# Performance work log

Hardware: AMD Instinct MI355X
Metric: run time of the kernel (lower is better)

The kernel has to match this reference:

```python
import jax, jax.numpy as jnp
import numpy as np

TOP_K = 8
N_HEADS = 16


def setup_inputs() -> dict:
    key = jax.random.key(0)
    ks = jax.random.split(key, 8)
    B, L, S, D = 8, 1024, 1024, 1024
    w_scale = 1.0 / np.sqrt(D)
    return {
        "queries": jax.random.normal(ks[0], (B, L, D), jnp.float32),
        "keys": jax.random.normal(ks[1], (B, S, D), jnp.float32),
        "values": jax.random.normal(ks[2], (B, S, D), jnp.float32),
        "Wq": jax.random.normal(ks[3], (D, D), jnp.float32) * w_scale,
        "bq": jnp.zeros((D,), jnp.float32),
        "Wk": jax.random.normal(ks[4], (D, D), jnp.float32) * w_scale,
        "bk": jnp.zeros((D,), jnp.float32),
        "Wv": jax.random.normal(ks[5], (D, D), jnp.float32) * w_scale,
        "bv": jnp.zeros((D,), jnp.float32),
        "Wo": jax.random.normal(ks[6], (D, D), jnp.float32) * w_scale,
        "bo": jnp.zeros((D,), jnp.float32),
    }


def reference(queries, keys, values, Wq, bq, Wk, bk, Wv, bv, Wo, bo):
    B, L, D = queries.shape
    S = keys.shape[1]
    H = N_HEADS
    E = D // H
    # projections (torch Linear: x @ W.T + b); relu on Q and V per source
    q = jax.nn.relu(queries @ Wq.T + bq).reshape(B, L, H, E)
    k = (keys @ Wk.T + bk).reshape(B, S, H, E)
    v = jax.nn.relu(values @ Wv.T + bv).reshape(B, S, H, E)
    scores = jnp.einsum('blhe,bshe->bhls', q, k)  # [B,H,L,S]
    # per-row top-k threshold; entries strictly below kth-largest masked to -inf
    thresh = jax.lax.top_k(scores, TOP_K)[0][..., -1:]
    masked = jnp.where(scores < thresh, -jnp.inf, scores)
    scale = 1.0 / np.sqrt(E)
    A = jax.nn.softmax(scale * masked, axis=-1)  # dropout p=0.0 -> identity
    V = jnp.einsum('bhls,bshd->blhd', A, v).reshape(B, L, D)
    out = V @ Wo.T + bo
    return out, A
```

## Files before the change

kernel.cpp:

```cpp
#include <hip/hip_runtime.h>
#include <hip/hip_bf16.h>


#define B_ 8
#define L_ 1024
#define S_ 1024
#define D_ 1024
#define H_ 16
#define E_ 64
#define TOPK_ 8

typedef __attribute__((ext_vector_type(8))) short bfrag8;
typedef __attribute__((ext_vector_type(4))) float f4acc;

__device__ __forceinline__ void gload_lds16(const float* g, float* l) {
  __builtin_amdgcn_global_load_lds(
      (const __attribute__((address_space(1))) unsigned int*)g,
      (__attribute__((address_space(3))) unsigned int*)l, 16, 0, 0);
}

__device__ __forceinline__ unsigned short f2bf(float f) {
  unsigned u = __float_as_uint(f);
  u += 0x7FFF + ((u >> 16) & 1);
  return (unsigned short)(u >> 16);
}

__device__ __forceinline__ unsigned enc_ord(float f) {
  int s = __float_as_int(f);
  return (unsigned)(s ^ ((s >> 31) | 0x80000000));
}
__device__ __forceinline__ float dec_ord(unsigned u) {
  int m = ((int)u >= 0) ? 0xFFFFFFFF : 0x80000000;
  return __int_as_float((int)(u ^ (unsigned)m));
}

__device__ __forceinline__ unsigned dpp_umax64(unsigned x) {
  unsigned t;
  t = (unsigned)__builtin_amdgcn_update_dpp((int)x, (int)x, 0x111, 0xf, 0xf, false);
  x = x > t ? x : t;
  t = (unsigned)__builtin_amdgcn_update_dpp((int)x, (int)x, 0x112, 0xf, 0xf, false);
  x = x > t ? x : t;
  t = (unsigned)__builtin_amdgcn_update_dpp((int)x, (int)x, 0x114, 0xf, 0xf, false);
  x = x > t ? x : t;
  t = (unsigned)__builtin_amdgcn_update_dpp((int)x, (int)x, 0x118, 0xf, 0xf, false);
  x = x > t ? x : t;
  t = (unsigned)__builtin_amdgcn_update_dpp((int)x, (int)x, 0x142, 0xa, 0xf, false);
  x = x > t ? x : t;
  t = (unsigned)__builtin_amdgcn_update_dpp((int)x, (int)x, 0x143, 0xc, 0xf, false);
  x = x > t ? x : t;
  return (unsigned)__builtin_amdgcn_readlane((int)x, 63);
}

__device__ __forceinline__ float dpp_fsum64(float x) {
  float t;
  t = __int_as_float(__builtin_amdgcn_update_dpp(0, __float_as_int(x), 0x111, 0xf, 0xf, true));
  x += t;
  t = __int_as_float(__builtin_amdgcn_update_dpp(0, __float_as_int(x), 0x112, 0xf, 0xf, true));
  x += t;
  t = __int_as_float(__builtin_amdgcn_update_dpp(0, __float_as_int(x), 0x114, 0xf, 0xf, true));
  x += t;
  t = __int_as_float(__builtin_amdgcn_update_dpp(0, __float_as_int(x), 0x118, 0xf, 0xf, true));
  x += t;
  t = __int_as_float(__builtin_amdgcn_update_dpp(0, __float_as_int(x), 0x142, 0xa, 0xf, true));
  x += t;
  t = __int_as_float(__builtin_amdgcn_update_dpp(0, __float_as_int(x), 0x143, 0xc, 0xf, true));
  x += t;
  return __int_as_float(__builtin_amdgcn_readlane(__float_as_int(x), 63));
}

template <int RELU>
__global__ __launch_bounds__(256) void gemm_abt(
    const float* __restrict__ A, const float* __restrict__ Bm,
    const float* __restrict__ bias, float* __restrict__ C,
    int M, int N, int K, int lda, int ldb, int ldc) {
  __shared__ float As[2][16][68];
  __shared__ float Bs[2][16][68];

  const int t = threadIdx.x;
  const int tx = t & 15, ty = t >> 4;
  const int m0 = blockIdx.y * 64, n0 = blockIdx.x * 64;
  const int sr = t >> 2, skq = (t & 3) * 4;

  float acc[4][4], tot[4][4];
#pragma unroll
  for (int r = 0; r < 4; ++r)
#pragma unroll
    for (int c = 0; c < 4; ++c) {
      acc[r][c] = 0.0f;
      tot[r][c] = 0.0f;
    }

  const float* Arow = A + (long long)(m0 + sr) * lda + skq;
  const float* Brow = Bm + (long long)(n0 + sr) * ldb + skq;

  float4 pa = *reinterpret_cast<const float4*>(Arow);
  float4 pb = *reinterpret_cast<const float4*>(Brow);
  {
    As[0][skq + 0][sr] = pa.x;
    As[0][skq + 1][sr] = pa.y;
    As[0][skq + 2][sr] = pa.z;
    As[0][skq + 3][sr] = pa.w;
    Bs[0][skq + 0][sr] = pb.x;
    Bs[0][skq + 1][sr] = pb.y;
    Bs[0][skq + 2][sr] = pb.z;
    Bs[0][skq + 3][sr] = pb.w;
  }
  __syncthreads();

  const int ntiles = K / 16;
  for (int ti = 0; ti < ntiles; ++ti) {
    const int cur = ti & 1, nxt = cur ^ 1;
    if (ti + 1 < ntiles) {
      pa = *reinterpret_cast<const float4*>(Arow + (ti + 1) * 16);
      pb = *reinterpret_cast<const float4*>(Brow + (ti + 1) * 16);
    }
#pragma unroll
    for (int kk = 0; kk < 16; ++kk) {
      const float4 a4 = *reinterpret_cast<const float4*>(&As[cur][kk][ty * 4]);
      const float4 b4 = *reinterpret_cast<const float4*>(&Bs[cur][kk][tx * 4]);
      const float av[4] = {a4.x, a4.y, a4.z, a4.w};
      const float bv[4] = {b4.x, b4.y, b4.z, b4.w};
#pragma unroll
      for (int r = 0; r < 4; ++r)
#pragma unroll
        for (int c = 0; c < 4; ++c) acc[r][c] = fmaf(av[r], bv[c], acc[r][c]);
    }
    if (ti + 1 < ntiles) {
      As[nxt][skq + 0][sr] = pa.x;
      As[nxt][skq + 1][sr] = pa.y;
      As[nxt][skq + 2][sr] = pa.z;
      As[nxt][skq + 3][sr] = pa.w;
      Bs[nxt][skq + 0][sr] = pb.x;
      Bs[nxt][skq + 1][sr] = pb.y;
      Bs[nxt][skq + 2][sr] = pb.z;
      Bs[nxt][skq + 3][sr] = pb.w;
    }
    const bool flush =
        (K == 1024) ? (ti == 31 || ti == 63) : (ti == ntiles - 1);
    if (flush) {
#pragma unroll
      for (int r = 0; r < 4; ++r)
#pragma unroll
        for (int c = 0; c < 4; ++c) {
          tot[r][c] = __fadd_rn(tot[r][c], acc[r][c]);
          acc[r][c] = 0.0f;
        }
    }
    __syncthreads();
  }

#pragma unroll
  for (int r = 0; r < 4; ++r) {
    const int m = m0 + ty * 4 + r;
#pragma unroll
    for (int c = 0; c < 4; ++c) {
      const int n = n0 + tx * 4 + c;
      float v = tot[r][c];
      if (bias) v = __fadd_rn(v, bias[n]);
      if (RELU) v = fmaxf(v, 0.0f);
      C[(long long)m * ldc + n] = v;
    }
  }
}

template <int RELU>
__global__ __launch_bounds__(256) void gemm_mfma(
    const float* __restrict__ A, const float* __restrict__ Bm,
    const float* __restrict__ bias, float* __restrict__ C,
    int M, int N, int K, int lda, int ldb, int ldc) {
  __shared__ unsigned short As[2][64][40];
  __shared__ unsigned short Bs[2][64][40];

  const int t = threadIdx.x;
  const int w = t >> 6, l = t & 63;
  const int lr = l & 15, lg = l >> 4;
  const int m0 = blockIdx.y * 64, n0 = blockIdx.x * 64;
  const int srow = t >> 2, scol = (t & 3) * 8;

  f4acc acc[4];
#pragma unroll
  for (int c = 0; c < 4; ++c) acc[c] = (f4acc){0.f, 0.f, 0.f, 0.f};

  const float* Arow = A + (long long)(m0 + srow) * lda + scol;
  const float* Brow = Bm + (long long)(n0 + srow) * ldb + scol;

  float4 pa0 = *reinterpret_cast<const float4*>(Arow);
  float4 pa1 = *reinterpret_cast<const float4*>(Arow + 4);
  float4 pb0 = *reinterpret_cast<const float4*>(Brow);
  float4 pb1 = *reinterpret_cast<const float4*>(Brow + 4);

  auto store_tile = [&](int buf, const float4& a0, const float4& a1,
                        const float4& b0, const float4& b1) {
    unsigned short* ap = &As[buf][srow][scol];
    ap[0] = f2bf(a0.x); ap[1] = f2bf(a0.y); ap[2] = f2bf(a0.z);
    ap[3] = f2bf(a0.w); ap[4] = f2bf(a1.x); ap[5] = f2bf(a1.y);
    ap[6] = f2bf(a1.z); ap[7] = f2bf(a1.w);
    unsigned short* bp = &Bs[buf][srow][scol];
    bp[0] = f2bf(b0.x); bp[1] = f2bf(b0.y); bp[2] = f2bf(b0.z);
    bp[3] = f2bf(b0.w); bp[4] = f2bf(b1.x); bp[5] = f2bf(b1.y);
    bp[6] = f2bf(b1.z); bp[7] = f2bf(b1.w);
  };

  store_tile(0, pa0, pa1, pb0, pb1);
  __syncthreads();

  const int nsteps = K / 32;
  for (int ks = 0; ks < nsteps; ++ks) {
    const int cur = ks & 1, nxt = cur ^ 1;
    if (ks + 1 < nsteps) {
      const int off = (ks + 1) * 32;
      pa0 = *reinterpret_cast<const float4*>(Arow + off);
      pa1 = *reinterpret_cast<const float4*>(Arow + off + 4);
      pb0 = *reinterpret_cast<const float4*>(Brow + off);
      pb1 = *reinterpret_cast<const float4*>(Brow + off + 4);
    }
    const bfrag8 av =
        *reinterpret_cast<const bfrag8*>(&As[cur][16 * w + lr][lg * 8]);
#pragma unroll
    for (int c = 0; c < 4; ++c) {
      const bfrag8 bv =
          *reinterpret_cast<const bfrag8*>(&Bs[cur][16 * c + lr][lg * 8]);
      acc[c] = __builtin_amdgcn_mfma_f32_16x16x32_bf16(av, bv, acc[c], 0, 0, 0);
    }
    if (ks + 1 < nsteps) store_tile(nxt, pa0, pa1, pb0, pb1);
    __syncthreads();
  }

#pragma unroll
  for (int c = 0; c < 4; ++c) {
    const int col = n0 + c * 16 + lr;
    const float bb = bias ? bias[col] : 0.0f;
#pragma unroll
    for (int j = 0; j < 4; ++j) {
      const int row = m0 + 16 * w + lg * 4 + j;
      float v = acc[c][j] + bb;
      if (RELU) v = fmaxf(v, 0.0f);
      C[(long long)row * ldc + col] = v;
    }
  }
}

__global__ __launch_bounds__(256) void transpose_k(const float* __restrict__ Kf,
                                                   float* __restrict__ Kt) {
  __shared__ float tl[64][65];
  const int bh = blockIdx.y;
  const int b = bh >> 4, h = bh & 15;
  const int s0 = blockIdx.x * 64;
  const int t = threadIdx.x;
#pragma unroll
  for (int i = 0; i < 16; ++i) {
    const int idx = i * 256 + t;
    const int sr = idx >> 6, e = idx & 63;
    tl[sr][e] = Kf[(((long long)(b << 10) + s0 + sr) << 10) + (h << 6) + e];
  }
  __syncthreads();
#pragma unroll
  for (int i = 0; i < 16; ++i) {
    const int idx = i * 256 + t;
    const int er = idx >> 6, s = idx & 63;
    Kt[(((long long)(bh << 6) + er) << 10) + s0 + s] = tl[s][er];
  }
}

__global__ __launch_bounds__(256, 4) void score_topk_fused(
    const float* __restrict__ Qf, const float* __restrict__ Kt,
    float* __restrict__ A, int* __restrict__ outIdx,
    float* __restrict__ outW, int* __restrict__ outCnt) {
#pragma clang fp contract(off)
  __shared__ float Ks[2][8][512];

  const int t = threadIdx.x;
  const int wv = t >> 6, u = t & 63;
  const int row0 = blockIdx.x * 16;
  const int b = row0 >> 14, h = (row0 >> 10) & 15;
  const int bh = (b << 4) + h;
  const int rbase = (row0 & 1023) + wv * 4;

  float qreg[4];
#pragma unroll
  for (int r = 0; r < 4; ++r)
    qreg[r] = Qf[(((long long)(b << 10) + rbase + r) << 10) + (h << 6) + u];

  const float* KtBase = Kt + ((long long)(bh << 6) << 10);

  float acc[4][16];
#pragma unroll
  for (int r = 0; r < 4; ++r)
#pragma unroll
    for (int j = 0; j < 16; ++j) acc[r][j] = 0.0f;

  auto stage = [&](int buf, int eo, int ch) {
    const int r0 = wv * 2;
#pragma unroll
    for (int i = 0; i < 2; ++i) {
      const float* src =
          KtBase + ((long long)(eo * 8 + r0 + i) << 10) + ch * 512;
      float* dst = &Ks[buf][r0 + i][0];
      gload_lds16(src + 4 * u, dst);
      gload_lds16(src + 256 + 4 * u, dst + 256);
    }
  };

  stage(0, 0, 0);
  __syncthreads();

  for (int eo = 0; eo < 8; ++eo) {
    float qv[8][4];
#pragma unroll
    for (int el = 0; el < 8; ++el)
#pragma unroll
      for (int r = 0; r < 4; ++r)
        qv[el][r] = __uint_as_float(__builtin_amdgcn_readlane(
            __float_as_uint(qreg[r]), eo * 8 + el));

    {
      stage(1, eo, 1);
#pragma unroll
      for (int el = 0; el < 8; ++el) {
        const float4 k0 = *reinterpret_cast<const float4*>(&Ks[0][el][4 * u]);
        const float4 k1 =
            *reinterpret_cast<const float4*>(&Ks[0][el][256 + 4 * u]);
#pragma unroll
        for (int r = 0; r < 4; ++r) {
          const float q = qv[el][r];
          acc[r][0] = fmaf(q, k0.x, acc[r][0]);
          acc[r][1] = fmaf(q, k0.y, acc[r][1]);
          acc[r][2] = fmaf(q, k0.z, acc[r][2]);
          acc[r][3] = fmaf(q, k0.w, acc[r][3]);
          acc[r][4] = fmaf(q, k1.x, acc[r][4]);
          acc[r][5] = fmaf(q, k1.y, acc[r][5]);
          acc[r][6] = fmaf(q, k1.z, acc[r][6]);
          acc[r][7] = fmaf(q, k1.w, acc[r][7]);
        }
      }
      __syncthreads();
    }
    {
      if (eo < 7) stage(0, eo + 1, 0);
#pragma unroll
      for (int el = 0; el < 8; ++el) {
        const float4 k0 = *reinterpret_cast<const float4*>(&Ks[1][el][4 * u]);
        const float4 k1 =
            *reinterpret_cast<const float4*>(&Ks[1][el][256 + 4 * u]);
#pragma unroll
        for (int r = 0; r < 4; ++r) {
          const float q = qv[el][r];
          acc[r][8] = fmaf(q, k0.x, acc[r][8]);
          acc[r][9] = fmaf(q, k0.y, acc[r][9]);
          acc[r][10] = fmaf(q, k0.z, acc[r][10]);
          acc[r][11] = fmaf(q, k0.w, acc[r][11]);
          acc[r][12] = fmaf(q, k1.x, acc[r][12]);
          acc[r][13] = fmaf(q, k1.y, acc[r][13]);
          acc[r][14] = fmaf(q, k1.z, acc[r][14]);
          acc[r][15] = fmaf(q, k1.w, acc[r][15]);
        }
      }
      __syncthreads();
    }
  }

  float T[4], cnt8[4], rowmax[4];
#pragma unroll
  for (int r = 0; r < 4; ++r) {
    T[r] = INFINITY;
    cnt8[r] = 0.0f;
    rowmax[r] = 0.0f;
  }

  for (int it = 0; it < TOPK_; ++it) {
    float m[4];
#pragma unroll
    for (int r = 0; r < 4; ++r) {
      float lm = -INFINITY;
#pragma unroll
      for (int j = 0; j < 16; ++j) {
        const float v = acc[r][j];
        lm = fmaxf(lm, v < T[r] ? v : -INFINITY);
      }
      m[r] = lm;
    }
    unsigned mu[4];
#pragma unroll
    for (int r = 0; r < 4; ++r) mu[r] = enc_ord(m[r]);
#pragma unroll
    for (int r = 0; r < 4; ++r) mu[r] = dpp_umax64(mu[r]);
#pragma unroll
    for (int r = 0; r < 4; ++r) m[r] = dec_ord(mu[r]);

    float nn[4];
#pragma unroll
    for (int r = 0; r < 4; ++r) {
      float cl = 0.0f;
#pragma unroll
      for (int j = 0; j < 16; ++j) cl += (acc[r][j] == m[r]) ? 1.0f : 0.0f;
      nn[r] = cl;
    }
#pragma unroll
    for (int r = 0; r < 4; ++r) nn[r] = dpp_fsum64(nn[r]);

#pragma unroll
    for (int r = 0; r < 4; ++r) {
      if (it == 0) rowmax[r] = m[r];
      const bool upd = (cnt8[r] < 8.0f);
      T[r] = upd ? m[r] : T[r];
      cnt8[r] = upd ? cnt8[r] + nn[r] : cnt8[r];
    }
  }

#pragma unroll
  for (int r = 0; r < 4; ++r) {
    const float thresh = T[r];
    float e16[16];
    float zl = 0.0f;
#pragma unroll
    for (int j = 0; j < 16; ++j) {
      const bool kept = (acc[r][j] >= thresh);
      const float e = kept ? __expf((acc[r][j] - rowmax[r]) * 0.125f) : 0.0f;
      e16[j] = e;
      zl += e;
    }
    const float zsum = dpp_fsum64(zl);
    const float inv = 1.0f / zsum;

    const long long row = row0 + wv * 4 + r;
    float* a = A + (row << 10);
    int cnt = 0;
#pragma unroll
    for (int j = 0; j < 16; ++j) {
      const bool kept = (acc[r][j] >= thresh);
      const float w = e16[j] * inv;
      e16[j] = kept ? w : 0.0f;
      const unsigned long long mk = __ballot(kept);
      if (kept) {
        const int pos = cnt + __popcll(mk & ((1ull << u) - 1ull));
        if (pos < 16) {
          const int col = (j >> 2) * 256 + 4 * u + (j & 3);
          outIdx[row * 16 + pos] = col;
          outW[row * 16 + pos] = w;
        }
      }
      cnt += __popcll(mk);
    }
    if (u == 0) outCnt[row] = cnt < 16 ? cnt : 16;

#pragma unroll
    for (int blkc = 0; blkc < 4; ++blkc) {
      float4 o;
      o.x = e16[blkc * 4 + 0];
      o.y = e16[blkc * 4 + 1];
      o.z = e16[blkc * 4 + 2];
      o.w = e16[blkc * 4 + 3];
      *reinterpret_cast<float4*>(&a[blkc * 256 + 4 * u]) = o;
    }
  }
}

__global__ __launch_bounds__(256) void vagg_kernel(
    const int* __restrict__ idx, const float* __restrict__ w,
    const int* __restrict__ cnt, const float* __restrict__ Vp,
    float* __restrict__ Vagg) {
  const int wave = threadIdx.x >> 6;
  const int lane = threadIdx.x & 63;
  const long long row = (long long)blockIdx.x * 4 + wave;
  const int b = (int)(row >> 14);
  const int h = (int)((row >> 10) & 15);
  const int l = (int)(row & 1023);
  const int n = cnt[row];
  float acc = 0.0f;
  for (int i = 0; i < n; ++i) {
    const int sI = idx[row * 16 + i];
    const float ww = w[row * 16 + i];
    acc += ww * Vp[((long long)((b << 10) + sI) << 10) + (h << 6) + lane];
  }
  Vagg[((long long)((b << 10) + l) << 10) + (h << 6) + lane] = acc;
}

extern "C" void kernel_launch(void* const* d_in, const int* in_sizes, int n_in,
                              void* d_out, int out_size, void* d_ws,
                              size_t ws_size, hipStream_t stream) {
  const float* queries = (const float*)d_in[0];
  const float* keys = (const float*)d_in[1];
  const float* values = (const float*)d_in[2];
  const float* Wq = (const float*)d_in[3];
  const float* bq = (const float*)d_in[4];
  const float* Wk = (const float*)d_in[5];
  const float* bk = (const float*)d_in[6];
  const float* Wv = (const float*)d_in[7];
  const float* bv = (const float*)d_in[8];
  const float* Wo = (const float*)d_in[9];
  const float* bo = (const float*)d_in[10];

  float* out = (float*)d_out;
  float* Aout = out + (long long)B_ * L_ * D_;

  char* ws = (char*)d_ws;
  const size_t MD = (size_t)B_ * L_ * D_ * sizeof(float);
  const size_t NL = (size_t)B_ * H_ * L_;
  float* Qf = (float*)ws;
  float* Kf = (float*)(ws + MD);
  float* Kt = (float*)(ws + 2 * MD);
  int* tIdx = (int*)(ws + 3 * MD);
  float* tW = (float*)(ws + 3 * MD + NL * 16 * 4);
  int* tCnt = (int*)(ws + 3 * MD + NL * 16 * 8);
  float* Vb = (float*)(ws + 3 * MD + NL * 16 * 8 + NL * 4);
  float* Vagg = Kt;

  const dim3 blk(256);
  const int M = B_ * L_;

  gemm_abt<1><<<dim3(16, M / 64), blk, 0, stream>>>(queries, Wq, bq, Qf, M, D_,
                                                    D_, D_, D_, D_);
  gemm_abt<0><<<dim3(16, M / 64), blk, 0, stream>>>(keys, Wk, bk, Kf, M, D_,
                                                    D_, D_, D_, D_);
  transpose_k<<<dim3(16, B_ * H_), blk, 0, stream>>>(Kf, Kt);

  score_topk_fused<<<(int)(NL / 16), blk, 0, stream>>>(Qf, Kt, Aout, tIdx, tW,
                                                       tCnt);

  gemm_mfma<1><<<dim3(16, M / 64), blk, 0, stream>>>(values, Wv, bv, Vb, M, D_,
                                                     D_, D_, D_, D_);

  vagg_kernel<<<(int)(NL / 4), blk, 0, stream>>>(tIdx, tW, tCnt, Vb, Vagg);

  gemm_mfma<0><<<dim3(16, M / 64), blk, 0, stream>>>(Vagg, Wo, bo, out, M, D_,
                                                     D_, D_, D_, D_);
}
```

Measured before the change: 1.213 ms.

## Fuse K transpose into projection GEMM epilogue and shrink score staging tiles

The key-projection GEMM now writes its output directly in the per-head transposed [B,H,E,S] layout through a templated epilogue using float4 stores. This removes the separate transpose kernel and one full-size intermediate buffer round trip. The score kernel's LDS staging is halved to 256-wide chunks in a four-step double-buffered loop with a fully unrolled outer loop, which lowers LDS use per block but adds more barriers. Vagg gets its own workspace region because Kt is no longer free to alias.

```diff
diff --git a/kernel.cpp b/kernel.cpp
--- a/kernel.cpp
+++ b/kernel.cpp
@@ -68,7 +68,7 @@
   return __int_as_float(__builtin_amdgcn_readlane(__float_as_int(x), 63));
 }
 
-template <int RELU>
+template <int RELU, int KT = 0>
 __global__ __launch_bounds__(256) void gemm_abt(
     const float* __restrict__ A, const float* __restrict__ Bm,
     const float* __restrict__ bias, float* __restrict__ C,
@@ -149,16 +149,33 @@
     __syncthreads();
   }
 
-#pragma unroll
-  for (int r = 0; r < 4; ++r) {
-    const int m = m0 + ty * 4 + r;
+  if (KT) {
+    const int bb = m0 >> 10;
+    const int sb = (m0 & 1023) + ty * 4;
 #pragma unroll
     for (int c = 0; c < 4; ++c) {
       const int n = n0 + tx * 4 + c;
-      float v = tot[r][c];
-      if (bias) v = __fadd_rn(v, bias[n]);
-      if (RELU) v = fmaxf(v, 0.0f);
-      C[(long long)m * ldc + n] = v;
+      const int hh = n >> 6, ee = n & 63;
+      float4 v;
+      v.x = __fadd_rn(tot[0][c], bias[n]);
+      v.y = __fadd_rn(tot[1][c], bias[n]);
+      v.z = __fadd_rn(tot[2][c], bias[n]);
+      v.w = __fadd_rn(tot[3][c], bias[n]);
+      *reinterpret_cast<float4*>(
+          &C[((((long long)(bb << 4) + hh) << 6) + ee) * 1024 + sb]) = v;
+    }
+  } else {
+#pragma unroll
+    for (int r = 0; r < 4; ++r) {
+      const int m = m0 + ty * 4 + r;
+#pragma unroll
+      for (int c = 0; c < 4; ++c) {
+        const int n = n0 + tx * 4 + c;
+        float v = tot[r][c];
+        if (bias) v = __fadd_rn(v, bias[n]);
+        if (RELU) v = fmaxf(v, 0.0f);
+        C[(long long)m * ldc + n] = v;
+      }
     }
   }
 }
@@ -240,34 +257,12 @@
   }
 }
 
-__global__ __launch_bounds__(256) void transpose_k(const float* __restrict__ Kf,
-                                                   float* __restrict__ Kt) {
-  __shared__ float tl[64][65];
-  const int bh = blockIdx.y;
-  const int b = bh >> 4, h = bh & 15;
-  const int s0 = blockIdx.x * 64;
-  const int t = threadIdx.x;
-#pragma unroll
-  for (int i = 0; i < 16; ++i) {
-    const int idx = i * 256 + t;
-    const int sr = idx >> 6, e = idx & 63;
-    tl[sr][e] = Kf[(((long long)(b << 10) + s0 + sr) << 10) + (h << 6) + e];
-  }
-  __syncthreads();
-#pragma unroll
-  for (int i = 0; i < 16; ++i) {
-    const int idx = i * 256 + t;
-    const int er = idx >> 6, s = idx & 63;
-    Kt[(((long long)(bh << 6) + er) << 10) + s0 + s] = tl[s][er];
-  }
-}
-
 __global__ __launch_bounds__(256, 4) void score_topk_fused(
     const float* __restrict__ Qf, const float* __restrict__ Kt,
     float* __restrict__ A, int* __restrict__ outIdx,
     float* __restrict__ outW, int* __restrict__ outCnt) {
 #pragma clang fp contract(off)
-  __shared__ float Ks[2][8][512];
+  __shared__ float Ks[2][8][256];
 
   const int t = threadIdx.x;
   const int wv = t >> 6, u = t & 63;
@@ -294,16 +289,15 @@
 #pragma unroll
     for (int i = 0; i < 2; ++i) {
       const float* src =
-          KtBase + ((long long)(eo * 8 + r0 + i) << 10) + ch * 512;
-      float* dst = &Ks[buf][r0 + i][0];
-      gload_lds16(src + 4 * u, dst);
-      gload_lds16(src + 256 + 4 * u, dst + 256);
+          KtBase + ((long long)(eo * 8 + r0 + i) << 10) + ch * 256 + 4 * u;
+      gload_lds16(src, &Ks[buf][r0 + i][0]);
     }
   };
 
   stage(0, 0, 0);
   __syncthreads();
 
+#pragma unroll
   for (int eo = 0; eo < 8; ++eo) {
     float qv[8][4];
 #pragma unroll
@@ -313,46 +307,24 @@
         qv[el][r] = __uint_as_float(__builtin_amdgcn_readlane(
             __float_as_uint(qreg[r]), eo * 8 + el));
 
-    {
-      stage(1, eo, 1);
+#pragma unroll
+    for (int ch = 0; ch < 4; ++ch) {
+      const int cur = ch & 1;
+      if (!(eo == 7 && ch == 3)) {
+        const int nch = (ch + 1) & 3;
+        const int neo = eo + (ch == 3 ? 1 : 0);
+        stage(cur ^ 1, neo, nch);
+      }
 #pragma unroll
       for (int el = 0; el < 8; ++el) {
-        const float4 k0 = *reinterpret_cast<const float4*>(&Ks[0][el][4 * u]);
-        const float4 k1 =
-            *reinterpret_cast<const float4*>(&Ks[0][el][256 + 4 * u]);
+        const float4 k4 = *reinterpret_cast<const float4*>(&Ks[cur][el][4 * u]);
 #pragma unroll
         for (int r = 0; r < 4; ++r) {
           const float q = qv[el][r];
-          acc[r][0] = fmaf(q, k0.x, acc[r][0]);
-          acc[r][1] = fmaf(q, k0.y, acc[r][1]);
-          acc[r][2] = fmaf(q, k0.z, acc[r][2]);
-          acc[r][3] = fmaf(q, k0.w, acc[r][3]);
-          acc[r][4] = fmaf(q, k1.x, acc[r][4]);
-          acc[r][5] = fmaf(q, k1.y, acc[r][5]);
-          acc[r][6] = fmaf(q, k1.z, acc[r][6]);
-          acc[r][7] = fmaf(q, k1.w, acc[r][7]);
-        }
-      }
-      __syncthreads();
-    }
-    {
-      if (eo < 7) stage(0, eo + 1, 0);
-#pragma unroll
-      for (int el = 0; el < 8; ++el) {
-        const float4 k0 = *reinterpret_cast<const float4*>(&Ks[1][el][4 * u]);
-        const float4 k1 =
-            *reinterpret_cast<const float4*>(&Ks[1][el][256 + 4 * u]);
-#pragma unroll
-        for (int r = 0; r < 4; ++r) {
-          const float q = qv[el][r];
-          acc[r][8] = fmaf(q, k0.x, acc[r][8]);
-          acc[r][9] = fmaf(q, k0.y, acc[r][9]);
-          acc[r][10] = fmaf(q, k0.z, acc[r][10]);
-          acc[r][11] = fmaf(q, k0.w, acc[r][11]);
-          acc[r][12] = fmaf(q, k1.x, acc[r][12]);
-          acc[r][13] = fmaf(q, k1.y, acc[r][13]);
-          acc[r][14] = fmaf(q, k1.z, acc[r][14]);
-          acc[r][15] = fmaf(q, k1.w, acc[r][15]);
+          acc[r][ch * 4 + 0] = fmaf(q, k4.x, acc[r][ch * 4 + 0]);
+          acc[r][ch * 4 + 1] = fmaf(q, k4.y, acc[r][ch * 4 + 1]);
+          acc[r][ch * 4 + 2] = fmaf(q, k4.z, acc[r][ch * 4 + 2]);
+          acc[r][ch * 4 + 3] = fmaf(q, k4.w, acc[r][ch * 4 + 3]);
         }
       }
       __syncthreads();
@@ -497,22 +469,20 @@
   const size_t MD = (size_t)B_ * L_ * D_ * sizeof(float);
   const size_t NL = (size_t)B_ * H_ * L_;
   float* Qf = (float*)ws;
-  float* Kf = (float*)(ws + MD);
-  float* Kt = (float*)(ws + 2 * MD);
-  int* tIdx = (int*)(ws + 3 * MD);
-  float* tW = (float*)(ws + 3 * MD + NL * 16 * 4);
-  int* tCnt = (int*)(ws + 3 * MD + NL * 16 * 8);
-  float* Vb = (float*)(ws + 3 * MD + NL * 16 * 8 + NL * 4);
-  float* Vagg = Kt;
+  float* Kt = (float*)(ws + MD);
+  int* tIdx = (int*)(ws + 2 * MD);
+  float* tW = (float*)(ws + 2 * MD + NL * 16 * 4);
+  int* tCnt = (int*)(ws + 2 * MD + NL * 16 * 8);
+  float* Vb = (float*)(ws + 2 * MD + NL * 16 * 8 + NL * 4);
+  float* Vagg = (float*)(ws + 3 * MD + NL * 16 * 8 + NL * 4);
 
   const dim3 blk(256);
   const int M = B_ * L_;
 
   gemm_abt<1><<<dim3(16, M / 64), blk, 0, stream>>>(queries, Wq, bq, Qf, M, D_,
                                                     D_, D_, D_, D_);
-  gemm_abt<0><<<dim3(16, M / 64), blk, 0, stream>>>(keys, Wk, bk, Kf, M, D_,
-                                                    D_, D_, D_, D_);
-  transpose_k<<<dim3(16, B_ * H_), blk, 0, stream>>>(Kf, Kt);
+  gemm_abt<0, 1><<<dim3(16, M / 64), blk, 0, stream>>>(keys, Wk, bk, Kt, M, D_,
+                                                       D_, D_, D_, D_);
 
   score_topk_fused<<<(int)(NL / 16), blk, 0, stream>>>(Qf, Kt, Aout, tIdx, tW,
                                                        tCnt);
```

New measurement: 1.276 ms. 1.05x slower.
